# Kernel optimization log

Measured on AMD Instinct MI355X. Metric: run time of the kernel, lower is better.

Reference implementation:

```python
import jax, jax.numpy as jnp
import numpy as np
from jax import lax

KH, KW = 9, 9
FC_DIM = 1024
C_RED = FC_DIM // 8  # 128
EPS = 1e-5


def conv_bn_relu(x, w, gamma, beta):
    # 3x3 conv, stride 1, pad 1 (NCHW / OIHW), then batch-stat BN + ReLU
    y = lax.conv_general_dilated(x, w, (1, 1), ((1, 1), (1, 1)),
                                 dimension_numbers=('NCHW', 'OIHW', 'NCHW'))
    mean = y.mean(axis=(0, 2, 3))
    var = y.var(axis=(0, 2, 3))
    y = (y - mean[None, :, None, None]) * lax.rsqrt(var + EPS)[None, :, None, None]
    y = y * gamma[None, :, None, None] + beta[None, :, None, None]
    return jnp.maximum(y, 0.0)


def local_weighting(feat, atten, kH, kW):
    # feat: [B,C,H,W]; atten: [B,H,W,kH*kW]
    # out[b,c,h,w] = sum_k atten[b,h,w,k] * feat_padded[b,c,h+dh_k,w+dw_k]
    B, C, H, W = feat.shape
    ph, pw = kH // 2, kW // 2
    fp = jnp.pad(feat, ((0, 0), (0, 0), (ph, ph), (pw, pw)))
    out = jnp.zeros_like(feat)
    k = 0
    for dh in range(kH):
        for dw in range(kW):
            out = out + fp[:, :, dh:dh + H, dw:dw + W] * atten[:, None, :, :, k]
            k += 1
    return out


def setup_inputs() -> dict:
    key = jax.random.key(0)
    ks = jax.random.split(key, 12)
    B, H, W = 4, 64, 64
    sc1 = 1.0 / np.sqrt(FC_DIM * 9)
    sc5 = 1.0 / np.sqrt(C_RED * 9)
    return {
        'low_key': jax.random.normal(ks[0], (B, FC_DIM, H, W), jnp.float32),
        'low_nonkey': jax.random.normal(ks[1], (B, FC_DIM, H, W), jnp.float32),
        'local_atten': jax.random.uniform(ks[2], (B, H, W, KH * KW), jnp.float32),
        'w1': jax.random.normal(ks[3], (C_RED, FC_DIM, 3, 3), jnp.float32) * sc1,
        'g1': jnp.ones((C_RED,), jnp.float32),
        'b1': jnp.zeros((C_RED,), jnp.float32),
        'w4': jax.random.normal(ks[4], (C_RED, FC_DIM, 3, 3), jnp.float32) * sc1,
        'g4': jnp.ones((C_RED,), jnp.float32),
        'b4': jnp.zeros((C_RED,), jnp.float32),
        'w5': jax.random.normal(ks[5], (C_RED, C_RED, 3, 3), jnp.float32) * sc5,
        'g5': jnp.ones((C_RED,), jnp.float32),
        'b5': jnp.zeros((C_RED,), jnp.float32),
        'fc1_w': jax.random.normal(ks[6], (10, C_RED), jnp.float32) * (1.0 / np.sqrt(C_RED)),
        'fc1_b': jnp.zeros((10,), jnp.float32),
        'fc2_w': jax.random.normal(ks[7], (1, 10), jnp.float32) * (1.0 / np.sqrt(10.0)),
        'fc2_b': jnp.zeros((1,), jnp.float32),
    }


def reference(low_key, low_nonkey, local_atten,
              w1, g1, b1, w4, g4, b4, w5, g5, b5,
              fc1_w, fc1_b, fc2_w, fc2_b):
    lk = conv_bn_relu(low_key, w1, g1, b1)          # [B,128,H,W]
    trans = local_weighting(lk, local_atten, KH, KW)
    lnk = conv_bn_relu(low_nonkey, w4, g4, b4)
    out = trans - lnk
    out = conv_bn_relu(out, w5, g5, b5)
    out = out.mean(axis=(2, 3))                      # adaptive avg pool to 1x1 -> [B,128]
    out = out @ fc1_w.T + fc1_b
    out = out @ fc2_w.T + fc2_b                      # [B,1]
    return out
```

## Files before the change

kernel.cpp:

```cpp
#include <hip/hip_runtime.h>
#include <hip/hip_bf16.h>


#define B_ 4
#define CM_ 128

typedef __attribute__((ext_vector_type(8))) short short8;
typedef __attribute__((ext_vector_type(4))) float floatx4;
typedef __attribute__((address_space(3))) unsigned lds_as;
typedef __attribute__((address_space(1))) const unsigned glb_as;

__device__ inline short f2bf(float f) {
  union { float f; unsigned u; } v; v.f = f;
  unsigned r = v.u + 0x7fff + ((v.u >> 16) & 1);
  return (short)(r >> 16);
}
__device__ inline float bf2f(unsigned short u) {
  union { unsigned u; float f; } v; v.u = ((unsigned)u) << 16;
  return v.f;
}

template <int KB>
__global__ void xprep_kernel(const float* __restrict__ x, short* __restrict__ xt) {
  int kb = blockIdx.x >> 4, rg = blockIdx.x & 15;
  int b = blockIdx.y;
  int row = rg * 4 + (threadIdx.x >> 6);
  int col = threadIdx.x & 63;
  const float* xs = x + (((size_t)b * (KB * 32) + kb * 32) * 64 + row) * 64 + col;
  short* xd = xt + ((((size_t)b * KB + kb) * 64 + row) * 64 + col) * 32;
  int sw = (col >> 1) & 3;
#pragma unroll
  for (int u = 0; u < 4; u++) {
    short8 pk;
#pragma unroll
    for (int j = 0; j < 8; j++) pk[j] = f2bf(xs[(size_t)(u * 8 + j) * 4096]);
    *(short8*)(xd + (u ^ sw) * 8) = pk;
  }
}

__global__ void prep1_kernel(const float* __restrict__ x1,
                             const float* __restrict__ w1, const float* __restrict__ w4,
                             const float* __restrict__ w5, const float* __restrict__ atten,
                             short* __restrict__ xt, short* __restrict__ wf1,
                             short* __restrict__ wf4, short* __restrict__ wf5,
                             float* __restrict__ att_t, float* __restrict__ yz) {
  __shared__ float tile[5184];
  int bx = blockIdx.x, tid = threadIdx.x;
  if (bx < 2048) {
    int b = bx & 3, t = bx >> 2;
    int kb = t >> 4, rg = t & 15;
    int row = rg * 4 + (tid >> 6), col = tid & 63;
    const float* xs = x1 + (((size_t)b * 1024 + kb * 32) * 64 + row) * 64 + col;
    short* xd = xt + ((((size_t)b * 32 + kb) * 64 + row) * 64 + col) * 32;
    int sw = (col >> 1) & 3;
#pragma unroll
    for (int u = 0; u < 4; u++) {
      short8 pk;
#pragma unroll
      for (int j = 0; j < 8; j++) pk[j] = f2bf(xs[(size_t)(u * 8 + j) * 4096]);
      *(short8*)(xd + (u ^ sw) * 8) = pk;
    }
    return;
  }
  bx -= 2048;
  if (bx < 1024) {
    const float* w = bx < 512 ? w1 : w4;
    short* wf = bx < 512 ? wf1 : wf4;
    int idx = (bx & 511) * 256 + tid;
    int oc = idx >> 10, ic = idx & 1023;
    int kb = ic >> 5, icb = ic & 31, quad = icb >> 3, j = icb & 7;
    int m = oc >> 4, n16 = oc & 15, lane = quad * 16 + n16;
    const float* wp = w + ((size_t)oc * 1024 + ic) * 9;
    short* base = wf + (size_t)kb * 36864 + lane * 8 + j;
#pragma unroll
    for (int r = 0; r < 3; r++)
#pragma unroll
      for (int s = 0; s < 3; s++)
        base[(size_t)r * 12288 + (s * 8 + m) * 512] = f2bf(wp[r * 3 + s]);
    return;
  }
  bx -= 1024;
  if (bx < 64) {
    int idx = bx * 256 + tid;
    int oc = idx >> 7, ic = idx & 127;
    int kb = ic >> 5, icb = ic & 31, quad = icb >> 3, j = icb & 7;
    int m = oc >> 4, n16 = oc & 15, lane = quad * 16 + n16;
    const float* wp = w5 + ((size_t)oc * 128 + ic) * 9;
    short* base = wf5 + (size_t)kb * 36864 + lane * 8 + j;
#pragma unroll
    for (int r = 0; r < 3; r++)
#pragma unroll
      for (int s = 0; s < 3; s++)
        base[(size_t)r * 12288 + (s * 8 + m) * 512] = f2bf(wp[r * 3 + s]);
    return;
  }
  bx -= 64;
  if (bx < 256) {
    int b = bx >> 6;
    int p0 = (bx & 63) * 64;
    const float* src = atten + ((size_t)b * 4096 + p0) * 81;
    for (int e = tid; e < 5184; e += 256) tile[e] = src[e];
    __syncthreads();
    for (int f = tid; f < 5184; f += 256) {
      int k = f >> 6, w_ = f & 63;
      att_t[((size_t)b * 81 + k) * 4096 + p0 + w_] = tile[w_ * 81 + k];
    }
    return;
  }
  bx -= 256;
  ((float4*)yz)[(size_t)bx * 256 + tid] = make_float4(0.f, 0.f, 0.f, 0.f);
}

template <int KQ, bool ATOMIC>
__global__ __launch_bounds__(256, 2)
void convm_kernel(const short* __restrict__ xt, const short* __restrict__ wf,
                  float* __restrict__ ya, float* __restrict__ yb, int KBtot) {
  __shared__ __attribute__((aligned(16))) short smem[32768];
  int tid = threadIdx.x, lane = tid & 63, wv = tid >> 6;
  int n16 = lane & 15, quad = lane >> 4;
  int pg = blockIdx.x;
  int b = pg >> 5, h0 = (pg & 31) * 2;
  int kb0 = blockIdx.y * KQ;
  int mh = wv & 1, nh = wv >> 1;
  float* yo = ATOMIC ? ya : (blockIdx.y ? yb : ya);
  short* sx = smem + 24576;

  if (h0 == 0)
    for (int i = tid; i < 1024; i += 256) ((int*)sx)[i] = 0;
  if (h0 == 62)
    for (int i = tid; i < 1024; i += 256) ((int*)(sx + 3 * 2048))[i] = 0;

  auto dma_x = [&](int kb) {
    int row = h0 - 1 + wv;
    if (row >= 0 && row < 64) {
      const short* src = xt + ((((size_t)b * KBtot + kb) * 64 + row) * 64) * 32 + lane * 8;
      short* dst = sx + wv * 2048 + lane * 8;
#pragma unroll
      for (int t = 0; t < 4; t++)
        __builtin_amdgcn_global_load_lds((glb_as*)(src + t * 512), (lds_as*)(dst + t * 512),
                                         16, 0, 0);
    }
  };
  auto dma_w = [&](int step, int buf) {
    const short* src = wf + ((size_t)kb0 * 3 + step) * 12288 + wv * 3072 + lane * 8;
    short* dst = smem + buf * 12288 + wv * 3072 + lane * 8;
#pragma unroll
    for (int t = 0; t < 6; t++)
      __builtin_amdgcn_global_load_lds((glb_as*)(src + t * 512), (lds_as*)(dst + t * 512),
                                       16, 0, 0);
  };

  floatx4 acc[4][4];
#pragma unroll
  for (int i = 0; i < 4; i++)
#pragma unroll
    for (int n = 0; n < 4; n++) acc[i][n] = (floatx4){0.f, 0.f, 0.f, 0.f};

  dma_x(kb0);
  dma_w(0, 0);
  const int NS = KQ * 3;
  for (int s = 0; s < NS; s++) {
    int r = s % 3;
    __syncthreads();
    if (r == 0 && s > 0) {
      dma_x(kb0 + s / 3);
      if (s + 1 < NS) dma_w(s + 1, (s + 1) & 1);
      __syncthreads();
    } else {
      if (s + 1 < NS) dma_w(s + 1, (s + 1) & 1);
    }
    const short* swb = smem + (s & 1) * 12288;
    int slot = nh + r;
    const short* sxr = sx + slot * 2048;
#pragma unroll
    for (int sp = 0; sp < 3; sp++) {
      short8 a[4];
#pragma unroll
      for (int i = 0; i < 4; i++)
        a[i] = *(const short8*)(swb + ((sp * 8 + mh * 4 + i) * 64 + lane) * 8);
#pragma unroll
      for (int n = 0; n < 4; n++) {
        int c = n * 16 + n16 + sp - 1;
        int cc = c < 0 ? 0 : (c > 63 ? 63 : c);
        short8 bf = *(const short8*)(sxr + cc * 32 + (quad ^ ((cc >> 1) & 3)) * 8);
        if ((n == 0 && sp == 0) || (n == 3 && sp == 2)) {
          short8 zz = {0, 0, 0, 0, 0, 0, 0, 0};
          bf = (c != cc) ? zz : bf;
        }
#pragma unroll
        for (int i = 0; i < 4; i++)
          acc[i][n] = __builtin_amdgcn_mfma_f32_16x16x32_bf16(a[i], bf, acc[i][n], 0, 0, 0);
      }
    }
  }

  int row = h0 + nh;
#pragma unroll
  for (int i = 0; i < 4; i++)
#pragma unroll
    for (int n = 0; n < 4; n++)
#pragma unroll
      for (int rg = 0; rg < 4; rg++) {
        int oc = mh * 64 + i * 16 + quad * 4 + rg;
        size_t gi = (((size_t)b * CM_ + oc) * 64 + row) * 64 + n * 16 + n16;
        if (ATOMIC)
          atomicAdd(&yo[gi], acc[i][n][rg]);
        else
          yo[gi] = acc[i][n][rg];
      }
}

__global__ void bnstats2_kernel(const float* __restrict__ y1, const float* __restrict__ g1,
                                const float* __restrict__ b1, float2* __restrict__ s1,
                                const float* __restrict__ y4, const float* __restrict__ g4,
                                const float* __restrict__ b4, float2* __restrict__ s4) {
  const float* y = blockIdx.y ? y4 : y1;
  const float* g = blockIdx.y ? g4 : g1;
  const float* bt = blockIdx.y ? b4 : b1;
  float2* scsh = blockIdx.y ? s4 : s1;
  int c = blockIdx.x;
  int tid = threadIdx.x;
  float s = 0.f, s2 = 0.f;
  for (int b = 0; b < B_; b++) {
    const float4* p = (const float4*)(y + ((size_t)(b * CM_) + c) * 4096);
    for (int i = tid; i < 1024; i += 256) {
      float4 v = p[i];
      s += v.x + v.y + v.z + v.w;
      s2 += v.x * v.x + v.y * v.y + v.z * v.z + v.w * v.w;
    }
  }
  for (int off = 32; off > 0; off >>= 1) {
    s += __shfl_down(s, off);
    s2 += __shfl_down(s2, off);
  }
  __shared__ float rs[4], rq[4];
  if ((tid & 63) == 0) { rs[tid >> 6] = s; rq[tid >> 6] = s2; }
  __syncthreads();
  if (tid == 0) {
    float S = rs[0] + rs[1] + rs[2] + rs[3];
    float Q = rq[0] + rq[1] + rq[2] + rq[3];
    float mean = S * (1.f / 16384.f);
    float var = Q * (1.f / 16384.f) - mean * mean;
    float sc = g[c] * rsqrtf(var + 1e-5f);
    scsh[c] = make_float2(sc, bt[c] - mean * sc);
  }
}

__global__ void bnstats_s2_kernel(const float* __restrict__ ya, const float* __restrict__ yb,
                                  const float* __restrict__ g, const float* __restrict__ bt,
                                  float2* __restrict__ scsh) {
  int c = blockIdx.x;
  int tid = threadIdx.x;
  float s = 0.f, s2 = 0.f;
  for (int b = 0; b < B_; b++) {
    const float4* p = (const float4*)(ya + ((size_t)(b * CM_) + c) * 4096);
    const float4* q = (const float4*)(yb + ((size_t)(b * CM_) + c) * 4096);
    for (int i = tid; i < 1024; i += 256) {
      float4 v = p[i], w = q[i];
      float a0 = v.x + w.x, a1 = v.y + w.y, a2 = v.z + w.z, a3 = v.w + w.w;
      s += a0 + a1 + a2 + a3;
      s2 += a0 * a0 + a1 * a1 + a2 * a2 + a3 * a3;
    }
  }
  for (int off = 32; off > 0; off >>= 1) {
    s += __shfl_down(s, off);
    s2 += __shfl_down(s2, off);
  }
  __shared__ float rs[4], rq[4];
  if ((tid & 63) == 0) { rs[tid >> 6] = s; rq[tid >> 6] = s2; }
  __syncthreads();
  if (tid == 0) {
    float S = rs[0] + rs[1] + rs[2] + rs[3];
    float Q = rq[0] + rq[1] + rq[2] + rq[3];
    float mean = S * (1.f / 16384.f);
    float var = Q * (1.f / 16384.f) - mean * mean;
    float sc = g[c] * rsqrtf(var + 1e-5f);
    scsh[c] = make_float2(sc, bt[c] - mean * sc);
  }
}

__global__ __launch_bounds__(256, 2)
void localw_kernel(const float* __restrict__ y1, const float2* __restrict__ scsh1,
                   const float* __restrict__ y4, const float2* __restrict__ scsh4,
                   const float* __restrict__ att_t, short* __restrict__ xt5) {
  __shared__ unsigned short lkb[16][12][72];
  int bx = blockIdx.x;
  int b = bx >> 4, h0 = (bx & 15) * 4;
  int cg = blockIdx.y;
  int tid = threadIdx.x;
  int lane = tid & 63;
  int wv = tid >> 6;

  for (int e = tid; e < 16 * 12 * 72; e += 256) {
    int c_l = e / (12 * 72);
    int rem = e % (12 * 72);
    int gri = rem / 72, j = rem % 72;
    int row = h0 - 4 + gri, col = j - 4;
    float v = 0.f;
    if (row >= 0 && row < 64 && col >= 0 && col < 64) {
      float2 ss = scsh1[cg * 16 + c_l];
      v = fmaxf(0.f, y1[((size_t)(b * CM_) + cg * 16 + c_l) * 4096 + row * 64 + col] * ss.x + ss.y);
    }
    lkb[c_l][gri][j] = (unsigned short)f2bf(v);
  }
  __syncthreads();

  float acc[4][4];
#pragma unroll
  for (int cc = 0; cc < 4; cc++)
#pragma unroll
    for (int h_i = 0; h_i < 4; h_i++) acc[cc][h_i] = 0.f;

  const float* ab = att_t + (size_t)b * 81 * 4096 + h0 * 64 + lane;

#pragma unroll
  for (int gri = 0; gri < 12; ++gri) {
    float win[4][9];
#pragma unroll
    for (int cc = 0; cc < 4; ++cc)
#pragma unroll
      for (int dw = 0; dw < 9; ++dw)
        win[cc][dw] = bf2f(lkb[wv * 4 + cc][gri][lane + dw]);
#pragma unroll
    for (int h_i = 0; h_i < 4; ++h_i) {
      int r = gri - h_i;
      if (r < 0 || r > 8) continue;
      const float* ap = ab + (size_t)(r * 9) * 4096 + h_i * 64;
      float a[9];
#pragma unroll
      for (int dw = 0; dw < 9; ++dw) a[dw] = ap[(size_t)dw * 4096];
#pragma unroll
      for (int cc = 0; cc < 4; ++cc)
#pragma unroll
        for (int dw = 0; dw < 9; ++dw)
          acc[cc][h_i] = fmaf(a[dw], win[cc][dw], acc[cc][h_i]);
    }
  }

#pragma unroll
  for (int cc = 0; cc < 4; ++cc) {
    int c = cg * 16 + wv * 4 + cc;
    float2 ss4 = scsh4[c];
    int icb = c & 31;
    int uu = (icb >> 3) ^ ((lane >> 1) & 3);
#pragma unroll
    for (int h_i = 0; h_i < 4; ++h_i) {
      int h = h0 + h_i;
      size_t gi = ((size_t)(b * CM_) + c) * 4096 + h * 64 + lane;
      float lnk = fmaxf(0.f, y4[gi] * ss4.x + ss4.y);
      float dv = acc[cc][h_i] - lnk;
      xt5[((((size_t)b * 4 + (c >> 5)) * 64 + h) * 64 + lane) * 32 + uu * 8 + (icb & 7)] =
          f2bf(dv);
    }
  }
}

__global__ void pool_kernel(const float* __restrict__ ya, const float* __restrict__ yb,
                            const float2* __restrict__ scsh, float* __restrict__ pooled) {
  int bc = blockIdx.x;
  int c = bc & 127;
  float2 ss = scsh[c];
  const float4* p = (const float4*)(ya + (size_t)bc * 4096);
  const float4* q = (const float4*)(yb + (size_t)bc * 4096);
  float s = 0.f;
  for (int i = threadIdx.x; i < 1024; i += 256) {
    float4 v = p[i], w = q[i];
    s += fmaxf(0.f, (v.x + w.x) * ss.x + ss.y) + fmaxf(0.f, (v.y + w.y) * ss.x + ss.y) +
         fmaxf(0.f, (v.z + w.z) * ss.x + ss.y) + fmaxf(0.f, (v.w + w.w) * ss.x + ss.y);
  }
  for (int off = 32; off > 0; off >>= 1) s += __shfl_down(s, off);
  __shared__ float rs[4];
  if ((threadIdx.x & 63) == 0) rs[threadIdx.x >> 6] = s;
  __syncthreads();
  if (threadIdx.x == 0) pooled[bc] = (rs[0] + rs[1] + rs[2] + rs[3]) * (1.f / 4096.f);
}

__global__ void fc_kernel(const float* __restrict__ pooled, const float* __restrict__ fc1w,
                          const float* __restrict__ fc1b, const float* __restrict__ fc2w,
                          const float* __restrict__ fc2b, float* __restrict__ out) {
  int lane = threadIdx.x;
  float p[B_][10];
#pragma unroll
  for (int b = 0; b < B_; b++)
#pragma unroll
    for (int j = 0; j < 10; j++) p[b][j] = 0.f;
  for (int c = lane; c < CM_; c += 64) {
#pragma unroll
    for (int b = 0; b < B_; b++) {
      float pv = pooled[b * CM_ + c];
#pragma unroll
      for (int j = 0; j < 10; j++) p[b][j] = fmaf(pv, fc1w[j * CM_ + c], p[b][j]);
    }
  }
  for (int off = 32; off > 0; off >>= 1)
#pragma unroll
    for (int b = 0; b < B_; b++)
#pragma unroll
      for (int j = 0; j < 10; j++) p[b][j] += __shfl_down(p[b][j], off);
  if (lane == 0) {
    for (int b = 0; b < B_; b++) {
      float o = fc2b[0];
      for (int j = 0; j < 10; j++) o += fc2w[j] * (p[b][j] + fc1b[j]);
      out[b] = o;
    }
  }
}

extern "C" void kernel_launch(void* const* d_in, const int* in_sizes, int n_in,
                              void* d_out, int out_size, void* d_ws, size_t ws_size,
                              hipStream_t stream) {
  const float* low_key    = (const float*)d_in[0];
  const float* low_nonkey = (const float*)d_in[1];
  const float* atten      = (const float*)d_in[2];
  const float* w1  = (const float*)d_in[3];
  const float* g1  = (const float*)d_in[4];
  const float* b1  = (const float*)d_in[5];
  const float* w4  = (const float*)d_in[6];
  const float* g4  = (const float*)d_in[7];
  const float* b4  = (const float*)d_in[8];
  const float* w5  = (const float*)d_in[9];
  const float* g5  = (const float*)d_in[10];
  const float* b5  = (const float*)d_in[11];
  const float* fc1w = (const float*)d_in[12];
  const float* fc1b = (const float*)d_in[13];
  const float* fc2w = (const float*)d_in[14];
  const float* fc2b = (const float*)d_in[15];

  char* w8 = (char*)d_ws;
  short* wf1   = (short*)w8;
  short* wf4   = (short*)(w8 + 2359296);
  short* wf5   = (short*)(w8 + 4718592);
  float* att_t = (float*)(w8 + 5308416);
  short* xt    = (short*)(w8 + 10616832);
  float* y1    = (float*)(w8 + 44171264);
  float* y4    = (float*)(w8 + 52559872);
  float2* scsh1 = (float2*)(w8 + 60948480);
  float2* scsh4 = scsh1 + CM_;
  float2* scsh5 = scsh4 + CM_;
  float* pooled = (float*)(scsh5 + CM_);
  short* xt5 = xt;
  float* out = (float*)d_out;

  prep1_kernel<<<7488, 256, 0, stream>>>(low_key, w1, w4, w5, atten,
                                         xt, wf1, wf4, wf5, att_t, y1);
  convm_kernel<8, true><<<dim3(128, 4), 256, 0, stream>>>(xt, wf1, y1, y1, 32);
  xprep_kernel<32><<<dim3(512, 4), 256, 0, stream>>>(low_nonkey, xt);
  convm_kernel<8, true><<<dim3(128, 4), 256, 0, stream>>>(xt, wf4, y4, y4, 32);
  bnstats2_kernel<<<dim3(128, 2), 256, 0, stream>>>(y1, g1, b1, scsh1, y4, g4, b4, scsh4);
  localw_kernel<<<dim3(64, 8), 256, 0, stream>>>(y1, scsh1, y4, scsh4, att_t, xt5);
  convm_kernel<2, false><<<dim3(128, 2), 256, 0, stream>>>(xt5, wf5, y1, y4, 4);
  bnstats_s2_kernel<<<128, 256, 0, stream>>>(y1, y4, g5, b5, scsh5);
  pool_kernel<<<512, 256, 0, stream>>>(y1, y4, scsh5, pooled);
  fc_kernel<<<1, 64, 0, stream>>>(pooled, fc1w, fc1b, fc2w, fc2b, out);
}
```

Baseline: 388.7 us.

## Deepen conv weight/input DMA pipeline with finer phases and explicit vmcnt waits

Rewrites the conv main loop as nine per-tap phases with a six-slot ring for weights prefetched four phases ahead and double-buffered input rows. It replaces __syncthreads with raw s_barrier plus explicit vmcnt waits, precomputes B-fragment LDS offsets, and raises MFMA priority with s_setprio. The goal is to hide global-to-LDS latency and cut barrier stalls. In exchange it uses more LDS (80KB), which may limit occupancy, and relies on hand-counted vmcnt values that are fragile.

```diff
diff --git a/kernel.cpp b/kernel.cpp
--- a/kernel.cpp
+++ b/kernel.cpp
@@ -18,6 +18,15 @@
 __device__ inline float bf2f(unsigned short u) {
   union { unsigned u; float f; } v; v.u = ((unsigned)u) << 16;
   return v.f;
+}
+
+template <int N> __device__ __forceinline__ void waitv() {
+  static_assert(N == 0 || N == 2 || N == 4 || N == 6 || N == 10, "bad vmcnt");
+  if constexpr (N == 0) asm volatile("s_waitcnt vmcnt(0)" ::: "memory");
+  else if constexpr (N == 2) asm volatile("s_waitcnt vmcnt(2)" ::: "memory");
+  else if constexpr (N == 4) asm volatile("s_waitcnt vmcnt(4)" ::: "memory");
+  else if constexpr (N == 6) asm volatile("s_waitcnt vmcnt(6)" ::: "memory");
+  else asm volatile("s_waitcnt vmcnt(10)" ::: "memory");
 }
 
 template <int KB>
@@ -115,7 +124,7 @@
 __global__ __launch_bounds__(256, 2)
 void convm_kernel(const short* __restrict__ xt, const short* __restrict__ wf,
                   float* __restrict__ ya, float* __restrict__ yb, int KBtot) {
-  __shared__ __attribute__((aligned(16))) short smem[32768];
+  __shared__ __attribute__((aligned(16))) short smem[40960];
   int tid = threadIdx.x, lane = tid & 63, wv = tid >> 6;
   int n16 = lane & 15, quad = lane >> 4;
   int pg = blockIdx.x;
@@ -123,78 +132,147 @@
   int kb0 = blockIdx.y * KQ;
   int mh = wv & 1, nh = wv >> 1;
   float* yo = ATOMIC ? ya : (blockIdx.y ? yb : ya);
-  short* sx = smem + 24576;
+  short* sx0 = smem + 24576;
 
   if (h0 == 0)
-    for (int i = tid; i < 1024; i += 256) ((int*)sx)[i] = 0;
+    for (int i = tid; i < 1024; i += 256) {
+      ((int*)sx0)[i] = 0;
+      ((int*)(sx0 + 8192))[i] = 0;
+    }
   if (h0 == 62)
-    for (int i = tid; i < 1024; i += 256) ((int*)(sx + 3 * 2048))[i] = 0;
-
-  auto dma_x = [&](int kb) {
-    int row = h0 - 1 + wv;
-    if (row >= 0 && row < 64) {
-      const short* src = xt + ((((size_t)b * KBtot + kb) * 64 + row) * 64) * 32 + lane * 8;
-      short* dst = sx + wv * 2048 + lane * 8;
-#pragma unroll
-      for (int t = 0; t < 4; t++)
-        __builtin_amdgcn_global_load_lds((glb_as*)(src + t * 512), (lds_as*)(dst + t * 512),
-                                         16, 0, 0);
-    }
-  };
-  auto dma_w = [&](int step, int buf) {
-    const short* src = wf + ((size_t)kb0 * 3 + step) * 12288 + wv * 3072 + lane * 8;
-    short* dst = smem + buf * 12288 + wv * 3072 + lane * 8;
-#pragma unroll
-    for (int t = 0; t < 6; t++)
-      __builtin_amdgcn_global_load_lds((glb_as*)(src + t * 512), (lds_as*)(dst + t * 512),
+    for (int i = tid; i < 1024; i += 256) {
+      ((int*)(sx0 + 3 * 2048))[i] = 0;
+      ((int*)(sx0 + 8192 + 3 * 2048))[i] = 0;
+    }
+
+  int row = h0 - 1 + wv;
+  int xw = __builtin_amdgcn_readfirstlane((row >= 0 && row < 64) ? 1 : 0);
+  const short* wfb = wf + (size_t)kb0 * 36864;
+
+  int boff[3][4];
+#pragma unroll
+  for (int sp = 0; sp < 3; sp++)
+#pragma unroll
+    for (int n = 0; n < 4; n++) {
+      int c = n * 16 + n16 + sp - 1;
+      int cc = c < 0 ? 0 : (c > 63 ? 63 : c);
+      boff[sp][n] = cc * 32 + (quad ^ ((cc >> 1) & 3)) * 8;
+    }
+  bool bz00 = (n16 == 0), bz32 = (n16 == 15);
+
+  floatx4 acc[4][4];
+#pragma unroll
+  for (int i = 0; i < 4; i++)
+#pragma unroll
+    for (int n = 0; n < 4; n++) acc[i][n] = (floatx4){0.f, 0.f, 0.f, 0.f};
+
+  if (xw) {
+    const short* xs = xt + ((((size_t)b * KBtot + kb0) * 64 + row) * 64) * 32 + lane * 8;
+    short* xd = sx0 + wv * 2048 + lane * 8;
+#pragma unroll
+    for (int t = 0; t < 4; t++)
+      __builtin_amdgcn_global_load_lds((glb_as*)(xs + t * 512), (lds_as*)(xd + t * 512),
                                        16, 0, 0);
-  };
-
-  floatx4 acc[4][4];
-#pragma unroll
-  for (int i = 0; i < 4; i++)
-#pragma unroll
-    for (int n = 0; n < 4; n++) acc[i][n] = (floatx4){0.f, 0.f, 0.f, 0.f};
-
-  dma_x(kb0);
-  dma_w(0, 0);
-  const int NS = KQ * 3;
-  for (int s = 0; s < NS; s++) {
-    int r = s % 3;
-    __syncthreads();
-    if (r == 0 && s > 0) {
-      dma_x(kb0 + s / 3);
-      if (s + 1 < NS) dma_w(s + 1, (s + 1) & 1);
-      __syncthreads();
-    } else {
-      if (s + 1 < NS) dma_w(s + 1, (s + 1) & 1);
-    }
-    const short* swb = smem + (s & 1) * 12288;
-    int slot = nh + r;
-    const short* sxr = sx + slot * 2048;
-#pragma unroll
-    for (int sp = 0; sp < 3; sp++) {
-      short8 a[4];
-#pragma unroll
-      for (int i = 0; i < 4; i++)
-        a[i] = *(const short8*)(swb + ((sp * 8 + mh * 4 + i) * 64 + lane) * 8);
-#pragma unroll
-      for (int n = 0; n < 4; n++) {
-        int c = n * 16 + n16 + sp - 1;
-        int cc = c < 0 ? 0 : (c > 63 ? 63 : c);
-        short8 bf = *(const short8*)(sxr + cc * 32 + (quad ^ ((cc >> 1) & 3)) * 8);
-        if ((n == 0 && sp == 0) || (n == 3 && sp == 2)) {
-          short8 zz = {0, 0, 0, 0, 0, 0, 0, 0};
-          bf = (c != cc) ? zz : bf;
-        }
-#pragma unroll
-        for (int i = 0; i < 4; i++)
-          acc[i][n] = __builtin_amdgcn_mfma_f32_16x16x32_bf16(a[i], bf, acc[i][n], 0, 0, 0);
-      }
-    }
-  }
-
-  int row = h0 + nh;
+  }
+#pragma unroll
+  for (int p = 0; p < 4; p++) {
+    const short* ws = wfb + (size_t)p * 4096 + wv * 1024 + lane * 8;
+    short* wd = smem + p * 4096 + wv * 1024 + lane * 8;
+    __builtin_amdgcn_global_load_lds((glb_as*)ws, (lds_as*)wd, 16, 0, 0);
+    __builtin_amdgcn_global_load_lds((glb_as*)(ws + 512), (lds_as*)(wd + 512), 16, 0, 0);
+  }
+  asm volatile("s_waitcnt lgkmcnt(0)" ::: "memory");
+  waitv<6>();
+  __builtin_amdgcn_s_barrier();
+
+#define PHASE(E, DO_W, DO_X, VX, VN, DO_TAIL)                                        \
+  {                                                                                  \
+    constexpr int rr_ = (E) / 3, sp_ = (E) % 3;                                      \
+    int ts_ = qp + (E); ts_ = ts_ >= 6 ? ts_ - 6 : ts_;                              \
+    const short* swt_ = smem + ts_ * 4096;                                           \
+    short8 a_[4];                                                                    \
+    _Pragma("unroll")                                                                \
+    for (int i = 0; i < 4; i++)                                                      \
+      a_[i] = *(const short8*)(swt_ + ((mh * 4 + i) * 64 + lane) * 8);               \
+    const short* sxr_ = sxread + (nh + rr_) * 2048;                                  \
+    short8 bf_[4];                                                                   \
+    _Pragma("unroll")                                                                \
+    for (int n = 0; n < 4; n++) {                                                    \
+      short8 bv = *(const short8*)(sxr_ + boff[sp_][n]);                             \
+      if ((n == 0 && sp_ == 0) || (n == 3 && sp_ == 2)) {                            \
+        short8 zz = {0, 0, 0, 0, 0, 0, 0, 0};                                        \
+        bool bz = (sp_ == 0) ? bz00 : bz32;                                          \
+        bv = bz ? zz : bv;                                                           \
+      }                                                                              \
+      bf_[n] = bv;                                                                   \
+    }                                                                                \
+    if (DO_W) {                                                                      \
+      int t2_ = qp + (E) + 4;                                                        \
+      t2_ = t2_ >= 12 ? t2_ - 12 : (t2_ >= 6 ? t2_ - 6 : t2_);                       \
+      const short* ws_ = wfb + (size_t)(9 * q + (E) + 4) * 4096 + wv * 1024 + lane * 8; \
+      short* wd_ = smem + t2_ * 4096 + wv * 1024 + lane * 8;                         \
+      __builtin_amdgcn_global_load_lds((glb_as*)ws_, (lds_as*)wd_, 16, 0, 0);        \
+      __builtin_amdgcn_global_load_lds((glb_as*)(ws_ + 512), (lds_as*)(wd_ + 512),   \
+                                       16, 0, 0);                                    \
+    }                                                                                \
+    if (DO_X) {                                                                      \
+      if (xw) {                                                                      \
+        const short* xs_ = xt +                                                      \
+            ((((size_t)b * KBtot + kb0 + q + 1) * 64 + row) * 64) * 32 + lane * 8;   \
+        short* xd_ = sxwr + wv * 2048 + lane * 8;                                    \
+        _Pragma("unroll")                                                            \
+        for (int t = 0; t < 4; t++)                                                  \
+          __builtin_amdgcn_global_load_lds((glb_as*)(xs_ + t * 512),                 \
+                                           (lds_as*)(xd_ + t * 512), 16, 0, 0);      \
+      }                                                                              \
+    }                                                                                \
+    __builtin_amdgcn_s_barrier();                                                    \
+    __builtin_amdgcn_s_setprio(1);                                                   \
+    _Pragma("unroll")                                                                \
+    for (int n = 0; n < 4; n++)                                                      \
+      _Pragma("unroll")                                                              \
+      for (int i = 0; i < 4; i++)                                                    \
+        acc[i][n] =                                                                  \
+            __builtin_amdgcn_mfma_f32_16x16x32_bf16(a_[i], bf_[n], acc[i][n], 0, 0, 0); \
+    __builtin_amdgcn_s_setprio(0);                                                   \
+    if (DO_TAIL) {                                                                   \
+      if ((VX) != (VN) && xw) { waitv<(VX)>(); } else { waitv<(VN)>(); }             \
+      __builtin_amdgcn_s_barrier();                                                  \
+    }                                                                                \
+  }
+
+  for (int q = 0; q < KQ - 1; ++q) {
+    int qp = (q & 1) * 3;
+    const short* sxread = sx0 + (q & 1) * 8192;
+    short* sxwr = sx0 + ((q + 1) & 1) * 8192;
+    PHASE(0, true, false, 6, 6, true)
+    PHASE(1, true, true, 10, 6, true)
+    PHASE(2, true, false, 10, 6, true)
+    PHASE(3, true, false, 10, 6, true)
+    PHASE(4, true, false, 10, 6, true)
+    PHASE(5, true, false, 6, 6, true)
+    PHASE(6, true, false, 6, 6, true)
+    PHASE(7, true, false, 6, 6, true)
+    PHASE(8, true, false, 6, 6, true)
+  }
+  {
+    const int q = KQ - 1;
+    int qp = (q & 1) * 3;
+    const short* sxread = sx0 + (q & 1) * 8192;
+    short* sxwr = nullptr; (void)sxwr;
+    PHASE(0, true, false, 6, 6, true)
+    PHASE(1, true, false, 6, 6, true)
+    PHASE(2, true, false, 6, 6, true)
+    PHASE(3, true, false, 6, 6, true)
+    PHASE(4, true, false, 6, 6, true)
+    PHASE(5, false, false, 4, 4, true)
+    PHASE(6, false, false, 2, 2, true)
+    PHASE(7, false, false, 0, 0, true)
+    PHASE(8, false, false, 0, 0, false)
+  }
+#undef PHASE
+
+  int orow = h0 + nh;
 #pragma unroll
   for (int i = 0; i < 4; i++)
 #pragma unroll
@@ -202,7 +280,7 @@
 #pragma unroll
       for (int rg = 0; rg < 4; rg++) {
         int oc = mh * 64 + i * 16 + quad * 4 + rg;
-        size_t gi = (((size_t)b * CM_ + oc) * 64 + row) * 64 + n * 16 + n16;
+        size_t gi = (((size_t)b * CM_ + oc) * 64 + orow) * 64 + n * 16 + n16;
         if (ATOMIC)
           atomicAdd(&yo[gi], acc[i][n][rg]);
         else
```

New measurement: 380.5 us. -2.1%, faster.

## Load conv weights straight to registers and double-buffer input rows in LDS

Applied to the files above, without the earlier changes.

The main conv kernel stops staging weight tiles through LDS. Each wave now loads its weight fragments directly from global memory into two alternating register sets, prefetching one phase ahead. Input rows are double-buffered in LDS and fetched one k-block ahead, so a block synchronises once per k-block instead of at every step. MFMA sections run at raised wave priority, and LDS use drops by half, which may allow higher occupancy. The cost is extra register pressure and weight loads from global/L2 that are no longer shared within the block, with only partial latency hiding.

```diff
diff --git a/kernel.cpp b/kernel.cpp
--- a/kernel.cpp
+++ b/kernel.cpp
@@ -18,6 +18,12 @@
 __device__ inline float bf2f(unsigned short u) {
   union { unsigned u; float f; } v; v.u = ((unsigned)u) << 16;
   return v.f;
+}
+
+__device__ __forceinline__ void kb_tail() {
+  asm volatile("s_waitcnt vmcnt(0)" ::: "memory");
+  __builtin_amdgcn_s_barrier();
+  asm volatile("" ::: "memory");
 }
 
 template <int KB>
@@ -115,7 +121,7 @@
 __global__ __launch_bounds__(256, 2)
 void convm_kernel(const short* __restrict__ xt, const short* __restrict__ wf,
                   float* __restrict__ ya, float* __restrict__ yb, int KBtot) {
-  __shared__ __attribute__((aligned(16))) short smem[32768];
+  __shared__ __attribute__((aligned(16))) short smem[16384];
   int tid = threadIdx.x, lane = tid & 63, wv = tid >> 6;
   int n16 = lane & 15, quad = lane >> 4;
   int pg = blockIdx.x;
@@ -123,78 +129,119 @@
   int kb0 = blockIdx.y * KQ;
   int mh = wv & 1, nh = wv >> 1;
   float* yo = ATOMIC ? ya : (blockIdx.y ? yb : ya);
-  short* sx = smem + 24576;
 
   if (h0 == 0)
-    for (int i = tid; i < 1024; i += 256) ((int*)sx)[i] = 0;
+    for (int i = tid; i < 1024; i += 256) {
+      ((int*)smem)[i] = 0;
+      ((int*)(smem + 8192))[i] = 0;
+    }
   if (h0 == 62)
-    for (int i = tid; i < 1024; i += 256) ((int*)(sx + 3 * 2048))[i] = 0;
-
-  auto dma_x = [&](int kb) {
-    int row = h0 - 1 + wv;
-    if (row >= 0 && row < 64) {
-      const short* src = xt + ((((size_t)b * KBtot + kb) * 64 + row) * 64) * 32 + lane * 8;
-      short* dst = sx + wv * 2048 + lane * 8;
-#pragma unroll
-      for (int t = 0; t < 4; t++)
-        __builtin_amdgcn_global_load_lds((glb_as*)(src + t * 512), (lds_as*)(dst + t * 512),
-                                         16, 0, 0);
-    }
-  };
-  auto dma_w = [&](int step, int buf) {
-    const short* src = wf + ((size_t)kb0 * 3 + step) * 12288 + wv * 3072 + lane * 8;
-    short* dst = smem + buf * 12288 + wv * 3072 + lane * 8;
-#pragma unroll
-    for (int t = 0; t < 6; t++)
-      __builtin_amdgcn_global_load_lds((glb_as*)(src + t * 512), (lds_as*)(dst + t * 512),
+    for (int i = tid; i < 1024; i += 256) {
+      ((int*)(smem + 3 * 2048))[i] = 0;
+      ((int*)(smem + 8192 + 3 * 2048))[i] = 0;
+    }
+
+  int xrow = h0 - 1 + wv;
+  int xw = __builtin_amdgcn_readfirstlane((xrow >= 0 && xrow < 64) ? 1 : 0);
+  const short* wfa = wf + (size_t)kb0 * 36864 + ((mh * 4) * 64 + lane) * 8;
+
+  int boff[3][4];
+#pragma unroll
+  for (int sp = 0; sp < 3; sp++)
+#pragma unroll
+    for (int n = 0; n < 4; n++) {
+      int c = n * 16 + n16 + sp - 1;
+      int cc = c < 0 ? 0 : (c > 63 ? 63 : c);
+      boff[sp][n] = cc * 32 + (quad ^ ((cc >> 1) & 3)) * 8;
+    }
+  bool bz00 = (n16 == 0), bz32 = (n16 == 15);
+
+  floatx4 acc[4][4];
+#pragma unroll
+  for (int i = 0; i < 4; i++)
+#pragma unroll
+    for (int n = 0; n < 4; n++) acc[i][n] = (floatx4){0.f, 0.f, 0.f, 0.f};
+
+  short8 AA[4], AB[4];
+
+  if (xw) {
+    const short* xs = xt + ((((size_t)b * KBtot + kb0) * 64 + xrow) * 64) * 32 + lane * 8;
+    short* xd = smem + wv * 2048 + lane * 8;
+#pragma unroll
+    for (int t = 0; t < 4; t++)
+      __builtin_amdgcn_global_load_lds((glb_as*)(xs + t * 512), (lds_as*)(xd + t * 512),
                                        16, 0, 0);
-  };
-
-  floatx4 acc[4][4];
-#pragma unroll
-  for (int i = 0; i < 4; i++)
-#pragma unroll
-    for (int n = 0; n < 4; n++) acc[i][n] = (floatx4){0.f, 0.f, 0.f, 0.f};
-
-  dma_x(kb0);
-  dma_w(0, 0);
-  const int NS = KQ * 3;
-  for (int s = 0; s < NS; s++) {
-    int r = s % 3;
-    __syncthreads();
-    if (r == 0 && s > 0) {
-      dma_x(kb0 + s / 3);
-      if (s + 1 < NS) dma_w(s + 1, (s + 1) & 1);
-      __syncthreads();
-    } else {
-      if (s + 1 < NS) dma_w(s + 1, (s + 1) & 1);
-    }
-    const short* swb = smem + (s & 1) * 12288;
-    int slot = nh + r;
-    const short* sxr = sx + slot * 2048;
-#pragma unroll
-    for (int sp = 0; sp < 3; sp++) {
-      short8 a[4];
-#pragma unroll
-      for (int i = 0; i < 4; i++)
-        a[i] = *(const short8*)(swb + ((sp * 8 + mh * 4 + i) * 64 + lane) * 8);
-#pragma unroll
-      for (int n = 0; n < 4; n++) {
-        int c = n * 16 + n16 + sp - 1;
-        int cc = c < 0 ? 0 : (c > 63 ? 63 : c);
-        short8 bf = *(const short8*)(sxr + cc * 32 + (quad ^ ((cc >> 1) & 3)) * 8);
-        if ((n == 0 && sp == 0) || (n == 3 && sp == 2)) {
-          short8 zz = {0, 0, 0, 0, 0, 0, 0, 0};
-          bf = (c != cc) ? zz : bf;
-        }
-#pragma unroll
-        for (int i = 0; i < 4; i++)
-          acc[i][n] = __builtin_amdgcn_mfma_f32_16x16x32_bf16(a[i], bf, acc[i][n], 0, 0, 0);
-      }
-    }
-  }
-
-  int row = h0 + nh;
+  }
+#pragma unroll
+  for (int i = 0; i < 4; i++) AA[i] = *(const short8*)(wfa + i * 512);
+  asm volatile("s_waitcnt lgkmcnt(0)" ::: "memory");
+  kb_tail();
+
+#define PH(QV, E, ACUR, ANXT, DONP, DOX, XB, DOTAIL)                                 \
+  {                                                                                  \
+    constexpr int rr_ = (E) / 3, sp_ = (E) % 3;                                      \
+    if (DONP) {                                                                      \
+      const short* ap_ = wfa + (size_t)(9 * (QV) + (E) + 1) * 4096;                  \
+      _Pragma("unroll")                                                              \
+      for (int i = 0; i < 4; i++) ANXT[i] = *(const short8*)(ap_ + i * 512);         \
+    }                                                                                \
+    if ((DOX) && xw) {                                                               \
+      const short* xs_ = xt +                                                        \
+          ((((size_t)b * KBtot + kb0 + (QV) + 1) * 64 + xrow) * 64) * 32 + lane * 8; \
+      short* xd_ = smem + (XB) * 8192 + wv * 2048 + lane * 8;                        \
+      _Pragma("unroll")                                                              \
+      for (int t = 0; t < 4; t++)                                                    \
+        __builtin_amdgcn_global_load_lds((glb_as*)(xs_ + t * 512),                   \
+                                         (lds_as*)(xd_ + t * 512), 16, 0, 0);        \
+    }                                                                                \
+    const short* sxr_ = smem + ((QV) & 1) * 8192 + (nh + rr_) * 2048;                \
+    short8 bf_[4];                                                                   \
+    _Pragma("unroll")                                                                \
+    for (int n = 0; n < 4; n++) {                                                    \
+      short8 bv = *(const short8*)(sxr_ + boff[sp_][n]);                             \
+      if ((n == 0 && sp_ == 0) || (n == 3 && sp_ == 2)) {                            \
+        short8 zz = {0, 0, 0, 0, 0, 0, 0, 0};                                        \
+        bv = ((sp_ == 0) ? bz00 : bz32) ? zz : bv;                                   \
+      }                                                                              \
+      bf_[n] = bv;                                                                   \
+    }                                                                                \
+    __builtin_amdgcn_s_setprio(1);                                                   \
+    _Pragma("unroll")                                                                \
+    for (int n = 0; n < 4; n++)                                                      \
+      _Pragma("unroll")                                                              \
+      for (int i = 0; i < 4; i++)                                                    \
+        acc[i][n] =                                                                  \
+            __builtin_amdgcn_mfma_f32_16x16x32_bf16(ACUR[i], bf_[n], acc[i][n], 0, 0, 0); \
+    __builtin_amdgcn_s_setprio(0);                                                   \
+    if (DOTAIL) kb_tail();                                                           \
+  }
+
+  const int NDQ = KQ / 2;
+  for (int dq = 0; dq < NDQ; ++dq) {
+    int q0 = 2 * dq, q1 = q0 + 1;
+    bool last = (dq == NDQ - 1);
+    PH(q0, 0, AA, AB, true, true, 1, false)
+    PH(q0, 1, AB, AA, true, false, 0, false)
+    PH(q0, 2, AA, AB, true, false, 0, false)
+    PH(q0, 3, AB, AA, true, false, 0, false)
+    PH(q0, 4, AA, AB, true, false, 0, false)
+    PH(q0, 5, AB, AA, true, false, 0, false)
+    PH(q0, 6, AA, AB, true, false, 0, false)
+    PH(q0, 7, AB, AA, true, false, 0, false)
+    PH(q0, 8, AA, AB, true, false, 0, true)
+    PH(q1, 0, AB, AA, true, !last, 0, false)
+    PH(q1, 1, AA, AB, true, false, 0, false)
+    PH(q1, 2, AB, AA, true, false, 0, false)
+    PH(q1, 3, AA, AB, true, false, 0, false)
+    PH(q1, 4, AB, AA, true, false, 0, false)
+    PH(q1, 5, AA, AB, true, false, 0, false)
+    PH(q1, 6, AB, AA, true, false, 0, false)
+    PH(q1, 7, AA, AB, true, false, 0, false)
+    PH(q1, 8, AB, AA, !last, false, 0, !last)
+  }
+#undef PH
+
+  int orow = h0 + nh;
 #pragma unroll
   for (int i = 0; i < 4; i++)
 #pragma unroll
@@ -202,7 +249,7 @@
 #pragma unroll
       for (int rg = 0; rg < 4; rg++) {
         int oc = mh * 64 + i * 16 + quad * 4 + rg;
-        size_t gi = (((size_t)b * CM_ + oc) * 64 + row) * 64 + n * 16 + n16;
+        size_t gi = (((size_t)b * CM_ + oc) * 64 + orow) * 64 + n * 16 + n16;
         if (ATOMIC)
           atomicAdd(&yo[gi], acc[i][n][rg]);
         else
```

Measured after the change: 384.3 us. No clear change (-1.1%).
